# Performance work log

Measured on AMD Instinct MI355X. Metric: run time of the kernel, lower is better.

## Reference

```python
import jax, jax.numpy as jnp
import numpy as np

B, T, D, H = 1, 2048, 1024, 16
HS = D // H  # 64
FF = 4 * D   # 4096
EPS = 1e-6


def rmsnorm(x, w):
    xf = x.astype(jnp.float32)
    n = xf * jax.lax.rsqrt(jnp.mean(xf * xf, axis=-1, keepdims=True) + EPS)
    return n.astype(x.dtype) * w


def setup_inputs() -> dict:
    key = jax.random.key(0)
    ks = jax.random.split(key, 9)
    s = 0.02
    return {
        "x": jax.random.normal(ks[0], (B, T, D), jnp.float32),
        "Wq": jax.random.normal(ks[1], (H, D, HS), jnp.float32) * s,
        "Wk": jax.random.normal(ks[2], (H, D, HS), jnp.float32) * s,
        "Wv": jax.random.normal(ks[3], (H, D, HS), jnp.float32) * s,
        "Wproj": jax.random.normal(ks[4], (H * HS, D), jnp.float32) * s,
        "bproj": jnp.zeros((D,), jnp.float32),
        "W1": jax.random.normal(ks[5], (D, FF), jnp.float32) * s,
        "W2": jax.random.normal(ks[6], (FF, D), jnp.float32) * s,
        "g1": jnp.ones((D,), jnp.float32),
        "g2": jnp.ones((D,), jnp.float32),
    }


def reference(x, Wq, Wk, Wv, Wproj, bproj, W1, W2, g1, g2):
    # --- self attention on RMSNorm(x) ---
    xn = rmsnorm(x, g1)                                   # [B,T,D]
    q = jnp.einsum('btd,hds->bhts', xn, Wq)               # [B,H,T,hs]
    k = jnp.einsum('btd,hds->bhts', xn, Wk)
    v = jnp.einsum('btd,hds->bhts', xn, Wv)
    scale = HS ** -0.5
    wei = jnp.einsum('bhts,bhus->bhtu', q, k) * scale     # [B,H,T,T]
    causal = jnp.tril(jnp.ones((T, T), bool))
    wei = jnp.where(causal, wei, -jnp.inf)
    wei = jax.nn.softmax(wei, axis=-1)
    attn = jnp.einsum('bhtu,bhus->bhts', wei, v)          # [B,H,T,hs]
    attn = attn.transpose(0, 2, 1, 3).reshape(B, T, H * HS)
    sa = attn @ Wproj + bproj                             # [B,T,D]
    x = x + sa
    # --- SiLU FFN on RMSNorm(x) ---
    xn2 = rmsnorm(x, g2)
    h = jax.nn.silu(xn2 @ W1)                             # [B,T,4D]
    x = x + h @ W2
    return x
```

## Files before the change

### kernel.cpp

```cpp
#include <hip/hip_runtime.h>

typedef unsigned short u16;
typedef unsigned int u32;
typedef __attribute__((ext_vector_type(4))) float f32x4;
typedef __attribute__((ext_vector_type(8))) __bf16 bf16x8;

#define T_SEQ 2048
#define DMODEL 1024
#define NHEAD 16
#define HEADS 64
#define FFDIM 4096
#define MNQ 2097152l

__device__ __forceinline__ u16 f2bf(float f) {
  u32 u = __builtin_bit_cast(u32, f);
  u = u + 0x7FFFu + ((u >> 16) & 1u);
  return (u16)(u >> 16);
}
__device__ __forceinline__ float bf2f(u16 h) {
  u32 u = ((u32)h) << 16;
  return __builtin_bit_cast(float, u);
}
__device__ __forceinline__ void gload_lds16(const u16* g, u16* l) {
  __builtin_amdgcn_global_load_lds(
      (const __attribute__((address_space(1))) u32*)g,
      (__attribute__((address_space(3))) u32*)l, 16, 0, 0);
}

__device__ __forceinline__ void transpose64(const float* __restrict__ in,
                                            long ldin, u16* __restrict__ out,
                                            long ldout, int r0, int c0, int tid,
                                            u16* tile) {
#pragma unroll
  for (int p = 0; p < 4; ++p) {
    int idx = p * 256 + tid;
    int r = idx >> 4, c4 = (idx & 15) * 4;
    float4 v = *(const float4*)(in + (long)(r0 + r) * ldin + c0 + c4);
    tile[(c4 + 0) * 66 + r] = f2bf(v.x);
    tile[(c4 + 1) * 66 + r] = f2bf(v.y);
    tile[(c4 + 2) * 66 + r] = f2bf(v.z);
    tile[(c4 + 3) * 66 + r] = f2bf(v.w);
  }
  __syncthreads();
#pragma unroll
  for (int p = 0; p < 2; ++p) {
    int idx = p * 256 + tid;
    int c = idx >> 3, rg = (idx & 7) * 8;
    u16 tmp[8];
#pragma unroll
    for (int j = 0; j < 8; ++j) tmp[j] = tile[c * 66 + rg + j];
    *(uint4*)(out + (long)(c0 + c) * ldout + r0 + rg) = *(uint4*)tmp;
  }
}

__global__ __launch_bounds__(256) void prep_k(
    const float* __restrict__ Wq, const float* __restrict__ Wk,
    const float* __restrict__ Wv, const float* __restrict__ Wproj,
    const float* __restrict__ x, const float* __restrict__ g1,
    u16* __restrict__ QKVwT, u16* __restrict__ WprojT, u16* __restrict__ xn1) {
  __shared__ u16 tile[64 * 66];
  __shared__ float wsum[4];
  int bid = blockIdx.x;
  int tid = threadIdx.x;
  if (bid >= 1024) {
    int row = bid - 1024;
    const float4* xr = (const float4*)(x + (long)row * DMODEL);
    float4 v = xr[tid];
    float ss = v.x * v.x + v.y * v.y + v.z * v.z + v.w * v.w;
#pragma unroll
    for (int off = 32; off >= 1; off >>= 1) ss += __shfl_xor(ss, off, 64);
    if ((tid & 63) == 0) wsum[tid >> 6] = ss;
    __syncthreads();
    float tot = wsum[0] + wsum[1] + wsum[2] + wsum[3];
    float rms = rsqrtf(tot * (1.0f / DMODEL) + 1e-6f);
    float4 gv = ((const float4*)g1)[tid];
    ushort4 o4 = make_ushort4(f2bf(v.x * rms * gv.x), f2bf(v.y * rms * gv.y),
                              f2bf(v.z * rms * gv.z), f2bf(v.w * rms * gv.w));
    ((ushort4*)(xn1 + (long)row * DMODEL))[tid] = o4;
    return;
  }
  const float* in;
  u16* out;
  long ldin, ldout;
  int r0, c0;
  if (bid < 768) {
    int z = bid >> 4, xi = bid & 15;
    int wsel = z >> 4, h = z & 15;
    in = (wsel == 0 ? Wq : (wsel == 1 ? Wk : Wv)) + (long)h * 65536;
    out = QKVwT + (long)wsel * 1048576 + (long)h * 65536;
    ldin = 64; ldout = 1024;
    r0 = xi * 64; c0 = 0;
  } else {
    int b = bid - 768;
    in = Wproj; out = WprojT; ldin = 1024; ldout = 1024;
    r0 = (b >> 4) * 64; c0 = (b & 15) * 64;
  }
  transpose64(in, ldin, out, ldout, r0, c0, tid, tile);
}

__global__ __launch_bounds__(256) void proj_rms_k(
    const u16* __restrict__ part, const float* __restrict__ bias,
    const float* __restrict__ resid, const float* __restrict__ g,
    float* __restrict__ x1, u16* __restrict__ xn2) {
  int row = blockIdx.x;
  int tid = threadIdx.x;
  long i = (long)row * DMODEL + tid * 4;
  float4 r = *(const float4*)(resid + i);
  float4 bi = *(const float4*)(bias + tid * 4);
  float4 v;
  v.x = r.x + bi.x; v.y = r.y + bi.y; v.z = r.z + bi.z; v.w = r.w + bi.w;
#pragma unroll
  for (int z = 0; z < 2; ++z) {
    ushort4 a = *(const ushort4*)(part + z * MNQ + i);
    v.x += bf2f(a.x); v.y += bf2f(a.y); v.z += bf2f(a.z); v.w += bf2f(a.w);
  }
  *(float4*)(x1 + i) = v;
  float ss = v.x * v.x + v.y * v.y + v.z * v.z + v.w * v.w;
#pragma unroll
  for (int off = 32; off >= 1; off >>= 1) ss += __shfl_xor(ss, off, 64);
  __shared__ float wsum[4];
  if ((tid & 63) == 0) wsum[tid >> 6] = ss;
  __syncthreads();
  float tot = wsum[0] + wsum[1] + wsum[2] + wsum[3];
  float rms = rsqrtf(tot * (1.0f / DMODEL) + 1e-6f);
  float4 gv = ((const float4*)g)[tid];
  ushort4 o4 = make_ushort4(f2bf(v.x * rms * gv.x), f2bf(v.y * rms * gv.y),
                            f2bf(v.z * rms * gv.z), f2bf(v.w * rms * gv.w));
  ((ushort4*)(xn2 + (long)row * DMODEL))[tid] = o4;
}

template <int EPI, int MODE, int NITER, bool FILL = false>
__global__ __launch_bounds__(256, 3) void gemm_bt_k(
    const u16* __restrict__ A, const u16* __restrict__ Bt, int N,
    u16* __restrict__ out16, u16* __restrict__ vt,
    u16* __restrict__ p0, u16* __restrict__ p1,
    const float* __restrict__ F1, const float* __restrict__ F2,
    u16* __restrict__ FT1, u16* __restrict__ FT2, int ngemm) {
  __shared__ __align__(16) u16 As[3][128 * 32];
  __shared__ __align__(16) u16 Bs[3][128 * 32];
  if constexpr (FILL) {
    if ((int)blockIdx.x >= ngemm) {
      int tb = (int)blockIdx.x - ngemm;
      u16* tile = (u16*)As;
      const float* in;
      u16* out;
      long ldin, ldout;
      int r0, c0;
      if (tb < 1024) {
        in = F1; out = FT1; ldin = 4096; ldout = 1024;
        r0 = (tb & 15) * 64; c0 = (tb >> 4) * 64;
      } else {
        int b = tb - 1024;
        in = F2; out = FT2; ldin = 1024; ldout = 4096;
        r0 = (b >> 4) * 64; c0 = (b & 15) * 64;
      }
      transpose64(in, ldin, out, ldout, r0, c0, threadIdx.x, tile);
      return;
    }
  }
  const int K = 1024 * ((EPI == 4 && MODE == 1) ? 4 : 1);
  const int kc = NITER * 32;
  int tid = threadIdx.x;
  int w = tid >> 6, lane = tid & 63;
  int quad = lane >> 4, l15 = lane & 15;
  int wr = w >> 1, wc = w & 1;

  int bid = blockIdx.x;
  int xcd = bid & 7, s = bid >> 3;
  int nn = N >> 7;
  int bx, by, kz;
  if (MODE == 0) {
    int nl = nn >> 3;
    by = xcd * nl + s % nl;
    int r = s / nl;
    bx = r & 15;
    kz = r >> 4;
  } else {
    bx = xcd * 2 + (s & 1);
    int r = s >> 1;
    by = r % nn;
    kz = r / nn;
  }
  int m0 = bx * 128, n0 = by * 128;

  f32x4 acc[4][4] = {};

  int lr = lane >> 2;
  int sw = (lr >> 1) & 3;
  int lc = ((lane & 3) ^ sw) * 8;
  const u16* Ak = A + (long)(m0 + w * 32 + lr) * K + lc + (long)kz * kc;
  const u16* A2k = Ak + (long)16 * K;
  const u16* Bk = Bt + (long)(n0 + w * 32 + lr) * K + lc + (long)kz * kc;
  const u16* B2k = Bk + (long)16 * K;

  gload_lds16(Ak, As[0] + w * 1024);
  gload_lds16(A2k, As[0] + w * 1024 + 512);
  gload_lds16(Bk, Bs[0] + w * 1024);
  gload_lds16(B2k, Bs[0] + w * 1024 + 512);
  gload_lds16(Ak + 32, As[1] + w * 1024);
  gload_lds16(A2k + 32, As[1] + w * 1024 + 512);
  gload_lds16(Bk + 32, Bs[1] + w * 1024);
  gload_lds16(B2k + 32, Bs[1] + w * 1024 + 512);

  int swq = (l15 >> 1) & 3;
  int qoff = (quad ^ swq) << 3;

#pragma unroll
  for (int k = 0; k < NITER; ++k) {
    const int cb = k % 3;
    if (k + 2 < NITER) {
      asm volatile("s_waitcnt vmcnt(4)\n\ts_barrier" ::: "memory");
      const int pb = (k + 2) % 3;
      const int off = (k + 2) * 32;
      gload_lds16(Ak + off, As[pb] + w * 1024);
      gload_lds16(A2k + off, As[pb] + w * 1024 + 512);
      gload_lds16(Bk + off, Bs[pb] + w * 1024);
      gload_lds16(B2k + off, Bs[pb] + w * 1024 + 512);
    } else {
      asm volatile("s_waitcnt vmcnt(0)\n\ts_barrier" ::: "memory");
    }
    const u16* Ab = As[cb];
    const u16* Bb = Bs[cb];
    bf16x8 af[4], bfr[4];
#pragma unroll
    for (int mt = 0; mt < 4; ++mt)
      af[mt] = *(const bf16x8*)(Ab + (wr * 64 + mt * 16 + l15) * 32 + qoff);
#pragma unroll
    for (int nt = 0; nt < 4; ++nt)
      bfr[nt] = *(const bf16x8*)(Bb + (wc * 64 + nt * 16 + l15) * 32 + qoff);
#pragma unroll
    for (int mt = 0; mt < 4; ++mt)
#pragma unroll
      for (int nt = 0; nt < 4; ++nt)
        acc[mt][nt] = __builtin_amdgcn_mfma_f32_16x16x32_bf16(
            af[mt], bfr[nt], acc[mt][nt], 0, 0, 0);
  }

  bool vblock = (EPI == 0) && (vt != nullptr) && (n0 >= 2048);
  u16* pb = nullptr;
  if (EPI == 4) pb = (kz < 4 ? p0 : p1) + (long)(kz & 3) * MNQ;
#pragma unroll
  for (int mt = 0; mt < 4; ++mt)
#pragma unroll
    for (int nt = 0; nt < 4; ++nt) {
      int col = n0 + wc * 64 + nt * 16 + l15;
      if (EPI == 0 && vblock) {
        int sc = col - 2048;
        int row0 = m0 + wr * 64 + mt * 16 + quad * 4;
        ushort4 pk = make_ushort4(f2bf(acc[mt][nt][0]), f2bf(acc[mt][nt][1]),
                                  f2bf(acc[mt][nt][2]), f2bf(acc[mt][nt][3]));
        *(ushort4*)(vt + (long)sc * 2048 + row0) = pk;
        continue;
      }
#pragma unroll
      for (int r = 0; r < 4; ++r) {
        int row = m0 + wr * 64 + mt * 16 + quad * 4 + r;
        long idx = (long)row * N + col;
        float v = acc[mt][nt][r];
        if (EPI == 0) {
          out16[idx] = f2bf(v);
        } else if (EPI == 2) {
          out16[idx] = f2bf(v / (1.0f + __expf(-v)));
        } else if (EPI == 4) {
          pb[idx] = f2bf(v);
        }
      }
    }
}

__global__ __launch_bounds__(256) void reduce_ffn2_k(
    const u16* __restrict__ p0, const float* __restrict__ resid,
    float* __restrict__ out) {
  long i = ((long)blockIdx.x * 256 + threadIdx.x) * 4;
  float4 r = *(const float4*)(resid + i);
  float4 o = r;
#pragma unroll
  for (int z = 0; z < 4; ++z) {
    ushort4 a = *(const ushort4*)(p0 + z * MNQ + i);
    o.x += bf2f(a.x);
    o.y += bf2f(a.y);
    o.z += bf2f(a.z);
    o.w += bf2f(a.w);
  }
  *(float4*)(out + i) = o;
}

#define LSTR 72
__global__ __launch_bounds__(256) void attn_part_k(const u16* __restrict__ QKV,
                                                   const u16* __restrict__ Vt,
                                                   u16* __restrict__ Opart,
                                                   float* __restrict__ lpart,
                                                   u16* __restrict__ attn) {
  __shared__ __align__(16) u16 Qs[64 * LSTR];
  __shared__ __align__(16) u16 Ks[64 * LSTR];
  __shared__ __align__(16) u16 Vs[64 * LSTR];
  __shared__ float lbuf[64];

  int tid = threadIdx.x;
  int w = tid >> 6, lane = tid & 63;
  int quad = lane >> 4, l15 = lane & 15;

  int bid = blockIdx.x;
  int xcd = bid & 7, sg = bid >> 3;
  int h = xcd * 2 + (sg & 1);
  int p = sg >> 1;

  int bx = 0, acc0 = 0;
  while (true) {
    int n = (bx >> 3) + 1;
    if (p < acc0 + n) break;
    acc0 += n;
    ++bx;
  }
  int c = p - acc0;
  int t0 = bx * 64;
  int jstart = c * 8;
  int jend = min(jstart + 8, bx + 1);

#pragma unroll
  for (int pp = 0; pp < 2; ++pp) {
    int idx = pp * 256 + tid;
    int row = idx >> 3, cc = idx & 7;
    *(uint4*)(Qs + row * LSTR + cc * 8) =
        *(const uint4*)(QKV + (long)(t0 + row) * 3072 + h * 64 + cc * 8);
  }
  __syncthreads();
  bf16x8 aq[2];
#pragma unroll
  for (int ks = 0; ks < 2; ++ks)
    aq[ks] = *(const bf16x8*)(Qs + (w * 16 + l15) * LSTR + ks * 32 + quad * 8);

  f32x4 oacc[4] = {};
  float lsum = 0.f;
  int qg = t0 + w * 16 + l15;

  u16* PsW = Qs + w * (16 * LSTR);

  for (int j = jstart; j < jend; ++j) {
    __syncthreads();
#pragma unroll
    for (int pp = 0; pp < 2; ++pp) {
      int idx = pp * 256 + tid;
      int row = idx >> 3, cc = idx & 7;
      *(uint4*)(Ks + row * LSTR + cc * 8) =
          *(const uint4*)(QKV + (long)(j * 64 + row) * 3072 + 1024 + h * 64 + cc * 8);
      *(uint4*)(Vs + row * LSTR + cc * 8) =
          *(const uint4*)(Vt + (long)h * (64 * 2048) + (long)row * 2048 + j * 64 + cc * 8);
    }
    __syncthreads();

    f32x4 sacc[4] = {};
#pragma unroll
    for (int ks = 0; ks < 2; ++ks)
#pragma unroll
      for (int ut = 0; ut < 4; ++ut) {
        bf16x8 kf = *(const bf16x8*)(Ks + (ut * 16 + l15) * LSTR + ks * 32 + quad * 8);
        sacc[ut] = __builtin_amdgcn_mfma_f32_16x16x32_bf16(kf, aq[ks], sacc[ut], 0, 0, 0);
      }

    bool boundary = (j == bx);
#pragma unroll
    for (int ut = 0; ut < 4; ++ut) {
      float pv[4];
#pragma unroll
      for (int r = 0; r < 4; ++r) {
        float v = exp2f(sacc[ut][r] * 0.18033688f);
        if (boundary) {
          int u = j * 64 + ut * 16 + quad * 4 + r;
          if (u > qg) v = 0.f;
        }
        pv[r] = v;
        lsum += v;
      }
      ushort4 pk = make_ushort4(f2bf(pv[0]), f2bf(pv[1]), f2bf(pv[2]), f2bf(pv[3]));
      *(ushort4*)(PsW + l15 * LSTR + ut * 16 + quad * 4) = pk;
    }
    asm volatile("s_waitcnt lgkmcnt(0)" ::: "memory");
#pragma unroll
    for (int ks = 0; ks < 2; ++ks) {
      bf16x8 pf = *(const bf16x8*)(PsW + l15 * LSTR + ks * 32 + quad * 8);
#pragma unroll
      for (int ct = 0; ct < 4; ++ct) {
        bf16x8 vf = *(const bf16x8*)(Vs + (ct * 16 + l15) * LSTR + ks * 32 + quad * 8);
        oacc[ct] = __builtin_amdgcn_mfma_f32_16x16x32_bf16(pf, vf, oacc[ct], 0, 0, 0);
      }
    }
  }

  lsum += __shfl_xor(lsum, 16, 64);
  lsum += __shfl_xor(lsum, 32, 64);
  if (quad == 0) lbuf[w * 16 + l15] = 1.0f / lsum;
  asm volatile("s_waitcnt lgkmcnt(0)" ::: "memory");

  float inv[4];
#pragma unroll
  for (int r = 0; r < 4; ++r) inv[r] = lbuf[w * 16 + quad * 4 + r];

  if (bx < 8) {
#pragma unroll
    for (int ct = 0; ct < 4; ++ct)
#pragma unroll
      for (int r = 0; r < 4; ++r)
        attn[(long)(t0 + w * 16 + quad * 4 + r) * 1024 + h * 64 + ct * 16 + l15] =
            f2bf(oacc[ct][r] * inv[r]);
    return;
  }
  long slot = (long)p * 16 + h;
  u16* Ob = Opart + slot * 4096;
#pragma unroll
  for (int ct = 0; ct < 4; ++ct)
#pragma unroll
    for (int r = 0; r < 4; ++r)
      Ob[(w * 16 + quad * 4 + r) * 64 + ct * 16 + l15] = f2bf(oacc[ct][r] * inv[r]);
  if (quad == 0) lpart[slot * 64 + w * 16 + l15] = lsum;
}

__global__ __launch_bounds__(256) void attn_combine_k(
    const u16* __restrict__ Opart, const float* __restrict__ lpart,
    u16* __restrict__ out) {
  int bx = blockIdx.x + 8, h = blockIdx.y;
  int g = bx >> 3;
  int p0 = 4 * g * (g + 1) + (bx - 8 * g) * (g + 1);
  int nc = g + 1;
  int tid = threadIdx.x;
  int row = tid >> 2, c4 = (tid & 3) * 16;

  float lv[4];
  float wsum = 0.f;
  for (int cidx = 0; cidx < nc; ++cidx) {
    long slot = (long)(p0 + cidx) * 16 + h;
    lv[cidx] = lpart[slot * 64 + row];
    wsum += lv[cidx];
  }
  float rinv = 1.0f / wsum;

  float o[16];
#pragma unroll
  for (int i = 0; i < 16; ++i) o[i] = 0.f;
  for (int cidx = 0; cidx < nc; ++cidx) {
    float wc = lv[cidx] * rinv;
    const u16* Ob = Opart + ((long)(p0 + cidx) * 16 + h) * 4096 + row * 64 + c4;
    bf16x8 a = *(const bf16x8*)Ob;
    bf16x8 b = *(const bf16x8*)(Ob + 8);
#pragma unroll
    for (int i = 0; i < 8; ++i) {
      o[i] += wc * (float)a[i];
      o[8 + i] += wc * (float)b[i];
    }
  }
  u16 ob[16];
#pragma unroll
  for (int i = 0; i < 16; ++i) ob[i] = f2bf(o[i]);
  u16* op = out + (long)(bx * 64 + row) * 1024 + h * 64 + c4;
  *(uint4*)op = *(uint4*)ob;
  *(uint4*)(op + 8) = *(uint4*)(ob + 8);
}

extern "C" void kernel_launch(void* const* d_in, const int* in_sizes, int n_in,
                              void* d_out, int out_size, void* d_ws, size_t ws_size,
                              hipStream_t stream) {
  const float* x     = (const float*)d_in[0];
  const float* Wq    = (const float*)d_in[1];
  const float* Wk    = (const float*)d_in[2];
  const float* Wv    = (const float*)d_in[3];
  const float* Wproj = (const float*)d_in[4];
  const float* bproj = (const float*)d_in[5];
  const float* W1    = (const float*)d_in[6];
  const float* W2    = (const float*)d_in[7];
  const float* g1    = (const float*)d_in[8];
  const float* g2    = (const float*)d_in[9];

  char* ws = (char*)d_ws;
  u16* QKVwT  = (u16*)(ws);
  u16* WprojT = (u16*)(ws + (6ul << 20));
  u16* W1T    = (u16*)(ws + (8ul << 20));
  u16* W2T    = (u16*)(ws + (16ul << 20));
  u16* xn1    = (u16*)(ws + (24ul << 20));
  u16* QKVb   = (u16*)(ws + (28ul << 20));
  u16* VtB    = (u16*)(ws + (40ul << 20));
  u16* attn   = (u16*)(ws + (44ul << 20));
  float* x1   = (float*)(ws + (48ul << 20));
  u16* xn2    = (u16*)(ws + (56ul << 20));
  u16* hbuf   = (u16*)(ws + (60ul << 20));
  u16* Opart    = (u16*)(ws + (48ul << 20));
  float* lpart  = (float*)(ws + (58ul << 20));
  u16* projp    = (u16*)(ws + (28ul << 20));
  u16* ffn2p    = (u16*)(ws + (28ul << 20));
  if (ws_size < (76ul << 20)) return;

  dim3 blk(256);

  prep_k<<<dim3(3072), blk, 0, stream>>>(
      Wq, Wk, Wv, Wproj, x, g1, QKVwT, WprojT, xn1);
  gemm_bt_k<0, 0, 32, true><<<dim3(2432), blk, 0, stream>>>(
      xn1, QKVwT, 3072, QKVb, VtB, nullptr, nullptr, W1, W2, W1T, W2T, 384);
  attn_part_k<<<dim3(1280), blk, 0, stream>>>(QKVb, VtB, Opart, lpart, attn);
  attn_combine_k<<<dim3(24, 16), blk, 0, stream>>>(Opart, lpart, attn);
  gemm_bt_k<4, 0, 16><<<dim3(256), blk, 0, stream>>>(
      attn, WprojT, 1024, nullptr, nullptr, projp, nullptr,
      nullptr, nullptr, nullptr, nullptr, 0);
  proj_rms_k<<<dim3(2048), blk, 0, stream>>>(projp, bproj, x, g2, x1, xn2);
  gemm_bt_k<2, 0, 32><<<dim3(512), blk, 0, stream>>>(
      xn2, W1T, 4096, hbuf, nullptr, nullptr, nullptr,
      nullptr, nullptr, nullptr, nullptr, 0);
  gemm_bt_k<4, 1, 32><<<dim3(512), blk, 0, stream>>>(
      hbuf, W2T, 1024, nullptr, nullptr, ffn2p, nullptr,
      nullptr, nullptr, nullptr, nullptr, 0);
  reduce_ffn2_k<<<dim3(2048), blk, 0, stream>>>(ffn2p, x1, (float*)d_out);
}
```

Before: 244.5 us.

## Add 512-thread 256x128-tile FFN GEMM kernel with 4-stage pipelined LDS loads

After: 248.0 us. Within noise of the previous version (+1.4%).

```diff
diff --git a/kernel.cpp b/kernel.cpp
--- a/kernel.cpp
+++ b/kernel.cpp
@@ -158,7 +158,7 @@
       return;
     }
   }
-  const int K = 1024 * ((EPI == 4 && MODE == 1) ? 4 : 1);
+  const int K = 1024;
   const int kc = NITER * 32;
   int tid = threadIdx.x;
   int w = tid >> 6, lane = tid & 63;
@@ -169,17 +169,12 @@
   int xcd = bid & 7, s = bid >> 3;
   int nn = N >> 7;
   int bx, by, kz;
-  if (MODE == 0) {
+  {
     int nl = nn >> 3;
     by = xcd * nl + s % nl;
     int r = s / nl;
     bx = r & 15;
     kz = r >> 4;
-  } else {
-    bx = xcd * 2 + (s & 1);
-    int r = s >> 1;
-    by = r % nn;
-    kz = r / nn;
   }
   int m0 = bx * 128, n0 = by * 128;
 
@@ -238,7 +233,7 @@
 
   bool vblock = (EPI == 0) && (vt != nullptr) && (n0 >= 2048);
   u16* pb = nullptr;
-  if (EPI == 4) pb = (kz < 4 ? p0 : p1) + (long)(kz & 3) * MNQ;
+  if (EPI == 4) pb = p0 + (long)kz * MNQ;
 #pragma unroll
   for (int mt = 0; mt < 4; ++mt)
 #pragma unroll
@@ -259,10 +254,128 @@
         float v = acc[mt][nt][r];
         if (EPI == 0) {
           out16[idx] = f2bf(v);
-        } else if (EPI == 2) {
-          out16[idx] = f2bf(v / (1.0f + __expf(-v)));
         } else if (EPI == 4) {
           pb[idx] = f2bf(v);
+        }
+      }
+    }
+}
+
+template <int EPI>
+__global__ __launch_bounds__(512, 1) void gemm8p_k(
+    const u16* __restrict__ A, const u16* __restrict__ Bt,
+    u16* __restrict__ out16, u16* __restrict__ pbuf) {
+  __shared__ __align__(16) u16 As[4 * 256 * 32];
+  __shared__ __align__(16) u16 Bs[4 * 128 * 32];
+  const int NT = 32;
+  const long Kst = (EPI == 4) ? 4096 : 1024;
+  const int N = (EPI == 4) ? 1024 : 4096;
+  int tid = threadIdx.x;
+  int w = tid >> 6, lane = tid & 63;
+  int quad = lane >> 4, l15 = lane & 15;
+  int wr = w >> 2, wc = w & 3;
+
+  int bid = blockIdx.x;
+  int xcd = bid & 7, s = bid >> 3;
+  int bx, by, kz;
+  if (EPI == 2) {
+    by = xcd * 4 + (s & 3);
+    bx = s >> 2;
+    kz = 0;
+  } else {
+    by = xcd;
+    bx = s & 7;
+    kz = s >> 3;
+  }
+  int m0 = bx * 256, n0 = by * 128;
+  long k0 = (long)kz * 1024;
+
+  f32x4 acc[8][2] = {};
+
+  const u16* Ag1 = A + (long)(m0 + (tid >> 2)) * Kst + k0 + (tid & 3) * 8;
+  const u16* Ag2 = Ag1 + (long)128 * Kst;
+  const u16* Bg = Bt + (long)(n0 + (tid >> 2)) * Kst + k0 + (tid & 3) * 8;
+  u16* Ald1 = As + w * 512;
+  u16* Ald2 = As + 4096 + w * 512;
+  u16* Bld = Bs + w * 512;
+
+#pragma unroll
+  for (int tt = 0; tt < 3; ++tt) {
+    gload_lds16(Ag1 + tt * 32, Ald1 + tt * 8192);
+    gload_lds16(Ag2 + tt * 32, Ald2 + tt * 8192);
+    gload_lds16(Bg + tt * 32, Bld + tt * 4096);
+  }
+  asm volatile("s_waitcnt vmcnt(6)\n\ts_barrier" ::: "memory");
+
+  const int arow = (wr * 128 + l15) * 32 + quad * 8;
+  const int brow = (wc * 32 + l15) * 32 + quad * 8;
+
+#pragma unroll
+  for (int t = 0; t < NT; ++t) {
+    const int cb = t & 3;
+    const u16* Ab = As + cb * 8192;
+    const u16* Bb = Bs + cb * 4096;
+    bf16x8 af[8], bf[2];
+#pragma unroll
+    for (int mt = 0; mt < 4; ++mt)
+      af[mt] = *(const bf16x8*)(Ab + arow + mt * 512);
+#pragma unroll
+    for (int nt = 0; nt < 2; ++nt)
+      bf[nt] = *(const bf16x8*)(Bb + brow + nt * 512);
+    if (t + 3 < NT) {
+      const int tb = (t + 3) & 3, off = (t + 3) * 32;
+      gload_lds16(Ag1 + off, Ald1 + tb * 8192);
+      gload_lds16(Ag2 + off, Ald2 + tb * 8192);
+    }
+    asm volatile("s_barrier" ::: "memory");
+    __builtin_amdgcn_s_setprio(1);
+#pragma unroll
+    for (int mt = 0; mt < 4; ++mt)
+#pragma unroll
+      for (int nt = 0; nt < 2; ++nt)
+        acc[mt][nt] = __builtin_amdgcn_mfma_f32_16x16x32_bf16(
+            af[mt], bf[nt], acc[mt][nt], 0, 0, 0);
+    __builtin_amdgcn_s_setprio(0);
+    asm volatile("s_barrier" ::: "memory");
+#pragma unroll
+    for (int mt = 4; mt < 8; ++mt)
+      af[mt] = *(const bf16x8*)(Ab + arow + mt * 512);
+    if (t + 3 < NT) {
+      const int tb = (t + 3) & 3, off = (t + 3) * 32;
+      gload_lds16(Bg + off, Bld + tb * 4096);
+      asm volatile("s_waitcnt vmcnt(6)\n\ts_barrier" ::: "memory");
+    } else if (t + 3 == NT) {
+      asm volatile("s_waitcnt vmcnt(3)\n\ts_barrier" ::: "memory");
+    } else if (t + 2 == NT) {
+      asm volatile("s_waitcnt vmcnt(0)\n\ts_barrier" ::: "memory");
+    } else {
+      asm volatile("s_barrier" ::: "memory");
+    }
+    __builtin_amdgcn_s_setprio(1);
+#pragma unroll
+    for (int mt = 4; mt < 8; ++mt)
+#pragma unroll
+      for (int nt = 0; nt < 2; ++nt)
+        acc[mt][nt] = __builtin_amdgcn_mfma_f32_16x16x32_bf16(
+            af[mt], bf[nt], acc[mt][nt], 0, 0, 0);
+    __builtin_amdgcn_s_setprio(0);
+    asm volatile("s_barrier" ::: "memory");
+  }
+
+  u16* pb = (EPI == 4) ? (pbuf + (long)kz * MNQ) : nullptr;
+#pragma unroll
+  for (int mt = 0; mt < 8; ++mt)
+#pragma unroll
+    for (int nt = 0; nt < 2; ++nt) {
+      int col = n0 + wc * 32 + nt * 16 + l15;
+#pragma unroll
+      for (int r = 0; r < 4; ++r) {
+        int row = m0 + wr * 128 + mt * 16 + quad * 4 + r;
+        float v = acc[mt][nt][r];
+        if (EPI == 2) {
+          out16[(long)row * N + col] = f2bf(v / (1.0f + __expf(-v)));
+        } else {
+          pb[(long)row * N + col] = f2bf(v);
         }
       }
     }
@@ -500,11 +613,7 @@
       attn, WprojT, 1024, nullptr, nullptr, projp, nullptr,
       nullptr, nullptr, nullptr, nullptr, 0);
   proj_rms_k<<<dim3(2048), blk, 0, stream>>>(projp, bproj, x, g2, x1, xn2);
-  gemm_bt_k<2, 0, 32><<<dim3(512), blk, 0, stream>>>(
-      xn2, W1T, 4096, hbuf, nullptr, nullptr, nullptr,
-      nullptr, nullptr, nullptr, nullptr, 0);
-  gemm_bt_k<4, 1, 32><<<dim3(512), blk, 0, stream>>>(
-      hbuf, W2T, 1024, nullptr, nullptr, ffn2p, nullptr,
-      nullptr, nullptr, nullptr, nullptr, 0);
+  gemm8p_k<2><<<dim3(256), dim3(512), 0, stream>>>(xn2, W1T, hbuf, nullptr);
+  gemm8p_k<4><<<dim3(256), dim3(512), 0, stream>>>(hbuf, W2T, nullptr, ffn2p);
   reduce_ffn2_k<<<dim3(2048), blk, 0, stream>>>(ffn2p, x1, (float*)d_out);
 }
```

## Load FFN GEMM operands straight from global to registers, bypassing LDS

Applied to the files above, without the earlier changes.

Result: slower. 316.6 us (+29.5%).

```diff
diff --git a/kernel.cpp b/kernel.cpp
--- a/kernel.cpp
+++ b/kernel.cpp
@@ -158,7 +158,114 @@
       return;
     }
   }
-  const int K = 1024 * ((EPI == 4 && MODE == 1) ? 4 : 1);
+  const int K = 1024;
+  const int kc = NITER * 32;
+  int tid = threadIdx.x;
+  int w = tid >> 6, lane = tid & 63;
+  int quad = lane >> 4, l15 = lane & 15;
+  int wr = w >> 1, wc = w & 1;
+
+  int bid = blockIdx.x;
+  int xcd = bid & 7, s = bid >> 3;
+  int nn = N >> 7;
+  int bx, by, kz;
+  {
+    int nl = nn >> 3;
+    by = xcd * nl + s % nl;
+    int r = s / nl;
+    bx = r & 15;
+    kz = r >> 4;
+  }
+  int m0 = bx * 128, n0 = by * 128;
+
+  f32x4 acc[4][4] = {};
+
+  int lr = lane >> 2;
+  int sw = (lr >> 1) & 3;
+  int lc = ((lane & 3) ^ sw) * 8;
+  const u16* Ak = A + (long)(m0 + w * 32 + lr) * K + lc + (long)kz * kc;
+  const u16* A2k = Ak + (long)16 * K;
+  const u16* Bk = Bt + (long)(n0 + w * 32 + lr) * K + lc + (long)kz * kc;
+  const u16* B2k = Bk + (long)16 * K;
+
+  gload_lds16(Ak, As[0] + w * 1024);
+  gload_lds16(A2k, As[0] + w * 1024 + 512);
+  gload_lds16(Bk, Bs[0] + w * 1024);
+  gload_lds16(B2k, Bs[0] + w * 1024 + 512);
+  gload_lds16(Ak + 32, As[1] + w * 1024);
+  gload_lds16(A2k + 32, As[1] + w * 1024 + 512);
+  gload_lds16(Bk + 32, Bs[1] + w * 1024);
+  gload_lds16(B2k + 32, Bs[1] + w * 1024 + 512);
+
+  int swq = (l15 >> 1) & 3;
+  int qoff = (quad ^ swq) << 3;
+
+#pragma unroll
+  for (int k = 0; k < NITER; ++k) {
+    const int cb = k % 3;
+    if (k + 2 < NITER) {
+      asm volatile("s_waitcnt vmcnt(4)\n\ts_barrier" ::: "memory");
+      const int pb = (k + 2) % 3;
+      const int off = (k + 2) * 32;
+      gload_lds16(Ak + off, As[pb] + w * 1024);
+      gload_lds16(A2k + off, As[pb] + w * 1024 + 512);
+      gload_lds16(Bk + off, Bs[pb] + w * 1024);
+      gload_lds16(B2k + off, Bs[pb] + w * 1024 + 512);
+    } else {
+      asm volatile("s_waitcnt vmcnt(0)\n\ts_barrier" ::: "memory");
+    }
+    const u16* Ab = As[cb];
+    const u16* Bb = Bs[cb];
+    bf16x8 af[4], bfr[4];
+#pragma unroll
+    for (int mt = 0; mt < 4; ++mt)
+      af[mt] = *(const bf16x8*)(Ab + (wr * 64 + mt * 16 + l15) * 32 + qoff);
+#pragma unroll
+    for (int nt = 0; nt < 4; ++nt)
+      bfr[nt] = *(const bf16x8*)(Bb + (wc * 64 + nt * 16 + l15) * 32 + qoff);
+#pragma unroll
+    for (int mt = 0; mt < 4; ++mt)
+#pragma unroll
+      for (int nt = 0; nt < 4; ++nt)
+        acc[mt][nt] = __builtin_amdgcn_mfma_f32_16x16x32_bf16(
+            af[mt], bfr[nt], acc[mt][nt], 0, 0, 0);
+  }
+
+  bool vblock = (EPI == 0) && (vt != nullptr) && (n0 >= 2048);
+  u16* pb = nullptr;
+  if (EPI == 4) pb = p0 + (long)kz * MNQ;
+#pragma unroll
+  for (int mt = 0; mt < 4; ++mt)
+#pragma unroll
+    for (int nt = 0; nt < 4; ++nt) {
+      int col = n0 + wc * 64 + nt * 16 + l15;
+      if (EPI == 0 && vblock) {
+        int sc = col - 2048;
+        int row0 = m0 + wr * 64 + mt * 16 + quad * 4;
+        ushort4 pk = make_ushort4(f2bf(acc[mt][nt][0]), f2bf(acc[mt][nt][1]),
+                                  f2bf(acc[mt][nt][2]), f2bf(acc[mt][nt][3]));
+        *(ushort4*)(vt + (long)sc * 2048 + row0) = pk;
+        continue;
+      }
+#pragma unroll
+      for (int r = 0; r < 4; ++r) {
+        int row = m0 + wr * 64 + mt * 16 + quad * 4 + r;
+        long idx = (long)row * N + col;
+        float v = acc[mt][nt][r];
+        if (EPI == 0) {
+          out16[idx] = f2bf(v);
+        } else if (EPI == 4) {
+          pb[idx] = f2bf(v);
+        }
+      }
+    }
+}
+
+template <int EPI, int MODE, int NITER>
+__global__ __launch_bounds__(256, 2) void gemm_direct_k(
+    const u16* __restrict__ A, const u16* __restrict__ Bt, int N,
+    u16* __restrict__ out16, u16* __restrict__ p0) {
+  const int K = (EPI == 4 && MODE == 1) ? 4096 : 1024;
   const int kc = NITER * 32;
   int tid = threadIdx.x;
   int w = tid >> 6, lane = tid & 63;
@@ -183,83 +290,59 @@
   }
   int m0 = bx * 128, n0 = by * 128;
 
+  const u16* Ap[4];
+  const u16* Bp[4];
+#pragma unroll
+  for (int mt = 0; mt < 4; ++mt)
+    Ap[mt] = A + (long)(m0 + wr * 64 + mt * 16 + l15) * K + (long)kz * kc + quad * 8;
+#pragma unroll
+  for (int nt = 0; nt < 4; ++nt)
+    Bp[nt] = Bt + (long)(n0 + wc * 64 + nt * 16 + l15) * K + (long)kz * kc + quad * 8;
+
   f32x4 acc[4][4] = {};
-
-  int lr = lane >> 2;
-  int sw = (lr >> 1) & 3;
-  int lc = ((lane & 3) ^ sw) * 8;
-  const u16* Ak = A + (long)(m0 + w * 32 + lr) * K + lc + (long)kz * kc;
-  const u16* A2k = Ak + (long)16 * K;
-  const u16* Bk = Bt + (long)(n0 + w * 32 + lr) * K + lc + (long)kz * kc;
-  const u16* B2k = Bk + (long)16 * K;
-
-  gload_lds16(Ak, As[0] + w * 1024);
-  gload_lds16(A2k, As[0] + w * 1024 + 512);
-  gload_lds16(Bk, Bs[0] + w * 1024);
-  gload_lds16(B2k, Bs[0] + w * 1024 + 512);
-  gload_lds16(Ak + 32, As[1] + w * 1024);
-  gload_lds16(A2k + 32, As[1] + w * 1024 + 512);
-  gload_lds16(Bk + 32, Bs[1] + w * 1024);
-  gload_lds16(B2k + 32, Bs[1] + w * 1024 + 512);
-
-  int swq = (l15 >> 1) & 3;
-  int qoff = (quad ^ swq) << 3;
+  bf16x8 ca[4], cb[4];
+#pragma unroll
+  for (int mt = 0; mt < 4; ++mt) ca[mt] = *(const bf16x8*)(Ap[mt]);
+#pragma unroll
+  for (int nt = 0; nt < 4; ++nt) cb[nt] = *(const bf16x8*)(Bp[nt]);
 
 #pragma unroll
   for (int k = 0; k < NITER; ++k) {
-    const int cb = k % 3;
-    if (k + 2 < NITER) {
-      asm volatile("s_waitcnt vmcnt(4)\n\ts_barrier" ::: "memory");
-      const int pb = (k + 2) % 3;
-      const int off = (k + 2) * 32;
-      gload_lds16(Ak + off, As[pb] + w * 1024);
-      gload_lds16(A2k + off, As[pb] + w * 1024 + 512);
-      gload_lds16(Bk + off, Bs[pb] + w * 1024);
-      gload_lds16(B2k + off, Bs[pb] + w * 1024 + 512);
-    } else {
-      asm volatile("s_waitcnt vmcnt(0)\n\ts_barrier" ::: "memory");
-    }
-    const u16* Ab = As[cb];
-    const u16* Bb = Bs[cb];
-    bf16x8 af[4], bfr[4];
-#pragma unroll
-    for (int mt = 0; mt < 4; ++mt)
-      af[mt] = *(const bf16x8*)(Ab + (wr * 64 + mt * 16 + l15) * 32 + qoff);
-#pragma unroll
-    for (int nt = 0; nt < 4; ++nt)
-      bfr[nt] = *(const bf16x8*)(Bb + (wc * 64 + nt * 16 + l15) * 32 + qoff);
+    bf16x8 na[4], nb[4];
+    if (k + 1 < NITER) {
+      const int off = (k + 1) * 32;
+#pragma unroll
+      for (int mt = 0; mt < 4; ++mt) na[mt] = *(const bf16x8*)(Ap[mt] + off);
+#pragma unroll
+      for (int nt = 0; nt < 4; ++nt) nb[nt] = *(const bf16x8*)(Bp[nt] + off);
+    }
 #pragma unroll
     for (int mt = 0; mt < 4; ++mt)
 #pragma unroll
       for (int nt = 0; nt < 4; ++nt)
         acc[mt][nt] = __builtin_amdgcn_mfma_f32_16x16x32_bf16(
-            af[mt], bfr[nt], acc[mt][nt], 0, 0, 0);
-  }
-
-  bool vblock = (EPI == 0) && (vt != nullptr) && (n0 >= 2048);
+            ca[mt], cb[nt], acc[mt][nt], 0, 0, 0);
+    if (k + 1 < NITER) {
+#pragma unroll
+      for (int mt = 0; mt < 4; ++mt) ca[mt] = na[mt];
+#pragma unroll
+      for (int nt = 0; nt < 4; ++nt) cb[nt] = nb[nt];
+    }
+  }
+
   u16* pb = nullptr;
-  if (EPI == 4) pb = (kz < 4 ? p0 : p1) + (long)(kz & 3) * MNQ;
+  if (EPI == 4) pb = p0 + (long)kz * MNQ;
 #pragma unroll
   for (int mt = 0; mt < 4; ++mt)
 #pragma unroll
     for (int nt = 0; nt < 4; ++nt) {
       int col = n0 + wc * 64 + nt * 16 + l15;
-      if (EPI == 0 && vblock) {
-        int sc = col - 2048;
-        int row0 = m0 + wr * 64 + mt * 16 + quad * 4;
-        ushort4 pk = make_ushort4(f2bf(acc[mt][nt][0]), f2bf(acc[mt][nt][1]),
-                                  f2bf(acc[mt][nt][2]), f2bf(acc[mt][nt][3]));
-        *(ushort4*)(vt + (long)sc * 2048 + row0) = pk;
-        continue;
-      }
 #pragma unroll
       for (int r = 0; r < 4; ++r) {
         int row = m0 + wr * 64 + mt * 16 + quad * 4 + r;
         long idx = (long)row * N + col;
         float v = acc[mt][nt][r];
-        if (EPI == 0) {
-          out16[idx] = f2bf(v);
-        } else if (EPI == 2) {
+        if (EPI == 2) {
           out16[idx] = f2bf(v / (1.0f + __expf(-v)));
         } else if (EPI == 4) {
           pb[idx] = f2bf(v);
@@ -500,11 +583,9 @@
       attn, WprojT, 1024, nullptr, nullptr, projp, nullptr,
       nullptr, nullptr, nullptr, nullptr, 0);
   proj_rms_k<<<dim3(2048), blk, 0, stream>>>(projp, bproj, x, g2, x1, xn2);
-  gemm_bt_k<2, 0, 32><<<dim3(512), blk, 0, stream>>>(
-      xn2, W1T, 4096, hbuf, nullptr, nullptr, nullptr,
-      nullptr, nullptr, nullptr, nullptr, 0);
-  gemm_bt_k<4, 1, 32><<<dim3(512), blk, 0, stream>>>(
-      hbuf, W2T, 1024, nullptr, nullptr, ffn2p, nullptr,
-      nullptr, nullptr, nullptr, nullptr, 0);
+  gemm_direct_k<2, 0, 32><<<dim3(512), blk, 0, stream>>>(
+      xn2, W1T, 4096, hbuf, nullptr);
+  gemm_direct_k<4, 1, 32><<<dim3(512), blk, 0, stream>>>(
+      hbuf, W2T, 1024, nullptr, ffn2p);
   reduce_ffn2_k<<<dim3(2048), blk, 0, stream>>>(ffn2p, x1, (float*)d_out);
 }
```
